# Kernel optimization log

Hardware: AMD Instinct MI355X
Metric: run time of the kernel (lower is better)

## Reference

```python
import jax, jax.numpy as jnp
import numpy as np

EMB = 2048
HEADS = 8
HEAD_DIM = EMB // HEADS  # 256

def setup_inputs() -> dict:
    key = jax.random.key(0)
    ks = jax.random.split(key, 4)
    b, n = 2, 2048
    x = jax.random.normal(ks[0], (b, n, EMB), dtype=jnp.float32)
    # Linear weights stored as [in, out] (y = x @ W + b)
    w_qkv = jax.random.normal(ks[1], (EMB, 3 * EMB), dtype=jnp.float32) * (EMB ** -0.5)
    b_qkv = jnp.zeros((3 * EMB,), dtype=jnp.float32)
    w_proj = jax.random.normal(ks[2], (EMB, EMB), dtype=jnp.float32) * (EMB ** -0.5)
    b_proj = jnp.zeros((EMB,), dtype=jnp.float32)
    return {"x": x, "w_qkv": w_qkv, "b_qkv": b_qkv, "w_proj": w_proj, "b_proj": b_proj}

def reference(x, w_qkv, b_qkv, w_proj, b_proj):
    b, n, _ = x.shape
    qkv = x @ w_qkv + b_qkv                                   # [b, n, 3*emb]
    # rearrange 'b n (h d qkv) -> qkv b h n d': qkv index is innermost
    qkv = qkv.reshape(b, n, HEADS, HEAD_DIM, 3)
    qkv = jnp.transpose(qkv, (4, 0, 2, 1, 3))                 # [3, b, h, n, d]
    q, k, v = qkv[0], qkv[1], qkv[2]
    energy = jnp.einsum('bhqd,bhkd->bhqk', q, k)              # [b, h, n, n]
    scaling = EMB ** 0.5
    # NOTE: faithful to source — softmax on UNSCALED logits, divide after.
    att = jax.nn.softmax(energy, axis=-1) / scaling
    out = jnp.einsum('bhal,bhlv->bhav', att, v)               # [b, h, n, d]
    out = jnp.transpose(out, (0, 2, 1, 3)).reshape(b, n, EMB)  # b n (h d)
    return out @ w_proj + b_proj
```

## Files before the change

kernel.cpp:

```cpp
#include <hip/hip_runtime.h>
#include <cstdint>
#include <cstddef>


typedef __bf16 bf16x8 __attribute__((ext_vector_type(8)));
typedef __bf16 bf16x2 __attribute__((ext_vector_type(2)));
typedef float f32x4 __attribute__((ext_vector_type(4)));

#define SCALE_INV 0.022097086912079608f

#define GLDS16(gp, lp)                                                        \
  __builtin_amdgcn_global_load_lds(                                           \
      (const __attribute__((address_space(1))) void*)(gp),                    \
      (__attribute__((address_space(3))) void*)(lp), 16, 0, 0)

__device__ inline void split8(const float4 v0, const float4 v1, bf16x8& hi,
                              bf16x8& lo) {
  float a[8] = {v0.x, v0.y, v0.z, v0.w, v1.x, v1.y, v1.z, v1.w};
  bf16x8 h, l;
#pragma unroll
  for (int i = 0; i < 8; i++) {
    __bf16 hh = (__bf16)a[i];
    h[i] = hh;
    l[i] = (__bf16)(a[i] - (float)hh);
  }
  hi = h;
  lo = l;
}

__global__ __launch_bounds__(256) void transpose_cvt_k(
    const float* __restrict__ in, __bf16* __restrict__ out, int R, int C) {
  __shared__ float tile[32][33];
  const int tx = threadIdx.x & 31;
  const int ty = threadIdx.x >> 5;
  const int c0 = blockIdx.x * 32;
  const int r0 = blockIdx.y * 32;
#pragma unroll
  for (int i = 0; i < 32; i += 8)
    tile[ty + i][tx] = in[(size_t)(r0 + ty + i) * C + (c0 + tx)];
  __syncthreads();
#pragma unroll
  for (int i = 0; i < 32; i += 8)
    out[(size_t)(c0 + ty + i) * R + (r0 + tx)] = (__bf16)tile[tx][ty + i];
}

__global__ __launch_bounds__(256) void transpose_w_split_k(
    const float* __restrict__ in, __bf16* __restrict__ wh,
    __bf16* __restrict__ wl1, __bf16* __restrict__ wl2) {
  __shared__ float tile[64][65];
  const int tid = threadIdx.x;
  const int c0 = blockIdx.x * 64;
  const int r0 = blockIdx.y * 64;
  const int cx = tid & 15, ry = tid >> 4;
#pragma unroll
  for (int p = 0; p < 4; p++) {
    const float4 v =
        *(const float4*)&in[(size_t)(r0 + p * 16 + ry) * 6144 + c0 + cx * 4];
    tile[p * 16 + ry][cx * 4 + 0] = v.x;
    tile[p * 16 + ry][cx * 4 + 1] = v.y;
    tile[p * 16 + ry][cx * 4 + 2] = v.z;
    tile[p * 16 + ry][cx * 4 + 3] = v.w;
  }
  __syncthreads();
  const int r2 = tid & 31;
  const int cy = tid >> 5;
  __bf16* wlb = (c0 < 2048) ? wl1 + (size_t)c0 * 2048
                            : wl2 + (size_t)(c0 - 2048) * 2048;
#pragma unroll
  for (int p = 0; p < 8; p++) {
    const int cl = cy + p * 8;
    const float t0 = tile[2 * r2][cl];
    const float t1 = tile[2 * r2 + 1][cl];
    const __bf16 h0 = (__bf16)t0, h1 = (__bf16)t1;
    bf16x2 hv = {h0, h1};
    bf16x2 lv = {(__bf16)(t0 - (float)h0), (__bf16)(t1 - (float)h1)};
    *(bf16x2*)&wh[(size_t)(c0 + cl) * 2048 + r0 + 2 * r2] = hv;
    *(bf16x2*)&wlb[(size_t)cl * 2048 + r0 + 2 * r2] = lv;
  }
}

__global__ __launch_bounds__(256) void gemm_qkv_split_k(
    const float* __restrict__ X, const __bf16* __restrict__ Wh,
    const __bf16* __restrict__ Wl1, const __bf16* __restrict__ Wl2,
    const float* __restrict__ bias, __bf16* __restrict__ qh_,
    __bf16* __restrict__ ql_, __bf16* __restrict__ kh_,
    __bf16* __restrict__ kl_, __bf16* __restrict__ vT) {
  __shared__ __bf16 Ah[2][128 * 40], Al[2][128 * 40];
  __shared__ __attribute__((aligned(16))) __bf16 BhL[2][4096];
  __shared__ __attribute__((aligned(16))) __bf16 BlL[2][4096];
  const int tid = threadIdx.x, lane = tid & 63, wave = tid >> 6;
  const int l16 = lane & 15, quad = lane >> 4;
  const int wm = (wave >> 1) * 64, wn = (wave & 1) * 64;
  const int m0 = blockIdx.y * 128, n0 = blockIdx.x * 128;
  const int r0 = tid >> 2, kc0 = (tid & 3) * 8;

  f32x4 zero4 = {0.f, 0.f, 0.f, 0.f};
  f32x4 acc[4][4];
#pragma unroll
  for (int i = 0; i < 4; i++)
#pragma unroll
    for (int j = 0; j < 4; j++) acc[i][j] = zero4;

  const float* Arow0 = X + (size_t)(m0 + r0) * 2048 + kc0;
  const float* Arow1 = Arow0 + (size_t)64 * 2048;
  const __bf16* BhP = Wh + (size_t)n0 * 2048;
  const __bf16* BlP = (n0 < 2048) ? Wl1 + (size_t)n0 * 2048
                                  : Wl2 + (size_t)(n0 - 2048) * 2048;

  const int rowl = lane >> 2, gq = lane & 3;
  const int sg = gq ^ (rowl & 3);
  size_t bSrc[2];
  int bDst[2];
#pragma unroll
  for (int i = 0; i < 2; i++) {
    const int row = wave * 32 + i * 16 + rowl;
    bSrc[i] = (size_t)row * 2048 + sg * 8;
    bDst[i] = (wave * 32 + i * 16) * 32;
  }
  const int bro = (wn + l16) * 32 + ((quad ^ (l16 & 3)) << 3);

  float4 a00 = *(const float4*)(Arow0);
  float4 a01 = *(const float4*)(Arow0 + 4);
  float4 a10 = *(const float4*)(Arow1);
  float4 a11 = *(const float4*)(Arow1 + 4);
  GLDS16(BhP + bSrc[0], &BhL[0][bDst[0]]);
  GLDS16(BhP + bSrc[1], &BhL[0][bDst[1]]);
  GLDS16(BlP + bSrc[0], &BlL[0][bDst[0]]);
  GLDS16(BlP + bSrc[1], &BlL[0][bDst[1]]);
  bf16x8 ah0, al0, ah1, al1;
  split8(a00, a01, ah0, al0);
  split8(a10, a11, ah1, al1);
  *(bf16x8*)&Ah[0][r0 * 40 + kc0] = ah0;
  *(bf16x8*)&Al[0][r0 * 40 + kc0] = al0;
  *(bf16x8*)&Ah[0][(r0 + 64) * 40 + kc0] = ah1;
  *(bf16x8*)&Al[0][(r0 + 64) * 40 + kc0] = al1;

  for (int k0 = 0; k0 < 2048; k0 += 32) {
    const int cur = (k0 >> 5) & 1;
    __syncthreads();
    const int nxt = k0 + 32;
    if (nxt < 2048) {
      a00 = *(const float4*)(Arow0 + nxt);
      a01 = *(const float4*)(Arow0 + nxt + 4);
      a10 = *(const float4*)(Arow1 + nxt);
      a11 = *(const float4*)(Arow1 + nxt + 4);
      GLDS16(BhP + bSrc[0] + nxt, &BhL[cur ^ 1][bDst[0]]);
      GLDS16(BhP + bSrc[1] + nxt, &BhL[cur ^ 1][bDst[1]]);
      GLDS16(BlP + bSrc[0] + nxt, &BlL[cur ^ 1][bDst[0]]);
      GLDS16(BlP + bSrc[1] + nxt, &BlL[cur ^ 1][bDst[1]]);
    }
    bf16x8 fah[4], fal[4], fbh[4], fbl[4];
#pragma unroll
    for (int i = 0; i < 4; i++) {
      fah[i] = *(const bf16x8*)&Ah[cur][(wm + i * 16 + l16) * 40 + quad * 8];
      fal[i] = *(const bf16x8*)&Al[cur][(wm + i * 16 + l16) * 40 + quad * 8];
    }
#pragma unroll
    for (int j = 0; j < 4; j++) {
      fbh[j] = *(const bf16x8*)&BhL[cur][bro + j * 512];
      fbl[j] = *(const bf16x8*)&BlL[cur][bro + j * 512];
    }
#pragma unroll
    for (int i = 0; i < 4; i++)
#pragma unroll
      for (int j = 0; j < 4; j++) {
        acc[i][j] = __builtin_amdgcn_mfma_f32_16x16x32_bf16(fah[i], fbh[j],
                                                            acc[i][j], 0, 0, 0);
        acc[i][j] = __builtin_amdgcn_mfma_f32_16x16x32_bf16(fah[i], fbl[j],
                                                            acc[i][j], 0, 0, 0);
        acc[i][j] = __builtin_amdgcn_mfma_f32_16x16x32_bf16(fal[i], fbh[j],
                                                            acc[i][j], 0, 0, 0);
      }
    if (nxt < 2048) {
      split8(a00, a01, ah0, al0);
      split8(a10, a11, ah1, al1);
      *(bf16x8*)&Ah[cur ^ 1][r0 * 40 + kc0] = ah0;
      *(bf16x8*)&Al[cur ^ 1][r0 * 40 + kc0] = al0;
      *(bf16x8*)&Ah[cur ^ 1][(r0 + 64) * 40 + kc0] = ah1;
      *(bf16x8*)&Al[cur ^ 1][(r0 + 64) * 40 + kc0] = al1;
    }
  }

#pragma unroll
  for (int i = 0; i < 4; i++) {
#pragma unroll
    for (int j = 0; j < 4; j++) {
      const int col = n0 + wn + j * 16 + l16;
      const float bv = bias[col];
      const int h = col / 768;
      const int rr = col - h * 768;
      const int d = rr / 3;
      const int c = rr - d * 3;
#pragma unroll
      for (int r = 0; r < 4; r++) {
        const int row = m0 + wm + i * 16 + quad * 4 + r;
        const float v = acc[i][j][r] + bv;
        const int b = row >> 11;
        const int nn = row & 2047;
        const int bh = b * 8 + h;
        const size_t idx = ((size_t)bh * 2048 + nn) * 256 + d;
        if (c == 0) {
          __bf16 hi = (__bf16)v;
          qh_[idx] = hi;
          ql_[idx] = (__bf16)(v - (float)hi);
        } else if (c == 1) {
          __bf16 hi = (__bf16)v;
          kh_[idx] = hi;
          kl_[idx] = (__bf16)(v - (float)hi);
        } else {
          vT[((size_t)bh * 256 + d) * 2048 + nn] = (__bf16)v;
        }
      }
    }
  }
}

__global__ __launch_bounds__(256, 2) void attn_fwd_k(
    const __bf16* __restrict__ Qh,
    const __bf16* __restrict__ Ql,
    const __bf16* __restrict__ Kh,
    const __bf16* __restrict__ Kl,
    const __bf16* __restrict__ Vt,
    __bf16* __restrict__ out) {
  __shared__ __attribute__((aligned(16))) __bf16 KhL[64 * 256];
  __shared__ __attribute__((aligned(16))) __bf16 KlL[64 * 256];
  __shared__ __attribute__((aligned(16))) __bf16 Plds[4][16 * 72];

  const int qblk = blockIdx.x;
  const int bh = blockIdx.y;
  const int bb = bh >> 3, hh = bh & 7;
  const int tid = threadIdx.x, lane = tid & 63, wave = tid >> 6;
  const int l16 = lane & 15, quad = lane >> 4;

  const size_t hqk = (size_t)bh * 2048 * 256;
  const __bf16* qhp = Qh + hqk;
  const __bf16* qlp = Ql + hqk;
  const __bf16* khp = Kh + hqk;
  const __bf16* klp = Kl + hqk;
  const __bf16* vp = Vt + (size_t)bh * 256 * 2048;

  const int qrow = qblk * 64 + wave * 16;

  bf16x8 qhf[8], qlf[8];
#pragma unroll
  for (int t = 0; t < 8; t++) {
    const size_t off = (size_t)(qrow + l16) * 256 + t * 32 + quad * 8;
    qhf[t] = *(const bf16x8*)&qhp[off];
    qlf[t] = *(const bf16x8*)&qlp[off];
  }

  f32x4 zero4 = {0.f, 0.f, 0.f, 0.f};
  f32x4 o[16];
#pragma unroll
  for (int dt = 0; dt < 16; dt++) o[dt] = zero4;
  float mrow[4], lrow[4];
#pragma unroll
  for (int r = 0; r < 4; r++) {
    mrow[r] = -3.0e38f;
    lrow[r] = 0.f;
  }

  int koff[8];
#pragma unroll
  for (int i = 0; i < 8; i++) {
    const int r = wave * 16 + i * 2 + (lane >> 5);
    const int cb = ((lane & 31) << 4) ^ ((r & 7) << 4);
    koff[i] = r * 256 + (cb >> 1);
  }
  const int ldsb = wave * 4096;

#pragma unroll
  for (int i = 0; i < 8; i++) {
    GLDS16(khp + koff[i], &KhL[ldsb + i * 512]);
    GLDS16(klp + koff[i], &KlL[ldsb + i * 512]);
  }

  for (int kv0 = 0; kv0 < 2048; kv0 += 64) {
    __syncthreads();

    f32x4 s[4];
#pragma unroll
    for (int j = 0; j < 4; j++) s[j] = zero4;
    __builtin_amdgcn_s_setprio(1);
#pragma unroll
    for (int j = 0; j < 4; j++) {
      const int row = j * 16 + l16;
      const int swz = (row & 7) << 3;
      const int rb = row * 256;
#pragma unroll
      for (int t = 0; t < 8; t++) {
        const int off = rb + ((t * 32 + quad * 8) ^ swz);
        bf16x8 khf = *(const bf16x8*)&KhL[off];
        bf16x8 klf = *(const bf16x8*)&KlL[off];
        s[j] =
            __builtin_amdgcn_mfma_f32_16x16x32_bf16(qhf[t], khf, s[j], 0, 0, 0);
        s[j] =
            __builtin_amdgcn_mfma_f32_16x16x32_bf16(qhf[t], klf, s[j], 0, 0, 0);
        s[j] =
            __builtin_amdgcn_mfma_f32_16x16x32_bf16(qlf[t], khf, s[j], 0, 0, 0);
      }
    }
    __builtin_amdgcn_s_setprio(0);
    __syncthreads();

    if (kv0 + 64 < 2048) {
      const int kvn = (kv0 + 64) * 256;
#pragma unroll
      for (int i = 0; i < 8; i++) {
        GLDS16(khp + kvn + koff[i], &KhL[ldsb + i * 512]);
        GLDS16(klp + kvn + koff[i], &KlL[ldsb + i * 512]);
      }
    }

    float mnew[4], alpha[4], psum[4];
#pragma unroll
    for (int r = 0; r < 4; r++) {
      float mx = fmaxf(fmaxf(s[0][r], s[1][r]), fmaxf(s[2][r], s[3][r]));
#pragma unroll
      for (int off = 1; off < 16; off <<= 1)
        mx = fmaxf(mx, __shfl_xor(mx, off, 16));
      mnew[r] = fmaxf(mrow[r], mx);
      alpha[r] = __expf(mrow[r] - mnew[r]);
      psum[r] = 0.f;
    }
#pragma unroll
    for (int j = 0; j < 4; j++)
#pragma unroll
      for (int r = 0; r < 4; r++) {
        float p = __expf(s[j][r] - mnew[r]);
        s[j][r] = p;
        psum[r] += p;
      }
#pragma unroll
    for (int r = 0; r < 4; r++) {
#pragma unroll
      for (int off = 1; off < 16; off <<= 1)
        psum[r] += __shfl_xor(psum[r], off, 16);
      lrow[r] = lrow[r] * alpha[r] + psum[r];
      mrow[r] = mnew[r];
    }
#pragma unroll
    for (int dt = 0; dt < 16; dt++) {
      o[dt][0] *= alpha[0];
      o[dt][1] *= alpha[1];
      o[dt][2] *= alpha[2];
      o[dt][3] *= alpha[3];
    }
#pragma unroll
    for (int j = 0; j < 4; j++)
#pragma unroll
      for (int r = 0; r < 4; r++)
        Plds[wave][(quad * 4 + r) * 72 + j * 16 + l16] = (__bf16)s[j][r];
    bf16x8 pa0 = *(const bf16x8*)&Plds[wave][l16 * 72 + quad * 8];
    bf16x8 pa1 = *(const bf16x8*)&Plds[wave][l16 * 72 + 32 + quad * 8];

    __builtin_amdgcn_s_setprio(1);
#pragma unroll
    for (int dt = 0; dt < 16; dt++) {
      const __bf16* vr = vp + (size_t)(dt * 16 + l16) * 2048 + kv0 + quad * 8;
      bf16x8 vf0 = *(const bf16x8*)vr;
      bf16x8 vf1 = *(const bf16x8*)(vr + 32);
      o[dt] = __builtin_amdgcn_mfma_f32_16x16x32_bf16(pa0, vf0, o[dt], 0, 0, 0);
      o[dt] = __builtin_amdgcn_mfma_f32_16x16x32_bf16(pa1, vf1, o[dt], 0, 0, 0);
    }
    __builtin_amdgcn_s_setprio(0);
  }

#pragma unroll
  for (int r = 0; r < 4; r++) {
    const float inv = SCALE_INV / lrow[r];
    const int n = qrow + quad * 4 + r;
    const size_t base = ((size_t)bb * 2048 + n) * 2048 + hh * 256;
#pragma unroll
    for (int dt = 0; dt < 16; dt++)
      out[base + dt * 16 + l16] = (__bf16)(o[dt][r] * inv);
  }
}

__global__ __launch_bounds__(256) void gemm_bt_k(
    const __bf16* __restrict__ A, const __bf16* __restrict__ Bt,
    const float* __restrict__ bias, int M, int Ncols, int K,
    float* __restrict__ outF) {
  __shared__ __bf16 As[128 * 40];
  __shared__ __bf16 Bs[128 * 40];
  const int tid = threadIdx.x, lane = tid & 63, wave = tid >> 6;
  const int l16 = lane & 15, quad = lane >> 4;
  const int wm = (wave >> 1) * 64, wn = (wave & 1) * 64;
  const int m0 = blockIdx.y * 128, n0 = blockIdx.x * 128;
  const int r0 = tid >> 2, kc0 = (tid & 3) * 8;

  f32x4 zero4 = {0.f, 0.f, 0.f, 0.f};
  f32x4 acc[4][4];
#pragma unroll
  for (int i = 0; i < 4; i++)
#pragma unroll
    for (int j = 0; j < 4; j++) acc[i][j] = zero4;

  const __bf16* Aptr = A + (size_t)(m0 + r0) * K + kc0;
  const __bf16* Bptr = Bt + (size_t)(n0 + r0) * K + kc0;
  const size_t rowstep = (size_t)64 * K;

  for (int k0 = 0; k0 < K; k0 += 32) {
    uint4 a0 = *(const uint4*)(Aptr + k0);
    uint4 a1 = *(const uint4*)(Aptr + rowstep + k0);
    uint4 b0 = *(const uint4*)(Bptr + k0);
    uint4 b1 = *(const uint4*)(Bptr + rowstep + k0);
    __syncthreads();
    *(uint4*)&As[r0 * 40 + kc0] = a0;
    *(uint4*)&As[(r0 + 64) * 40 + kc0] = a1;
    *(uint4*)&Bs[r0 * 40 + kc0] = b0;
    *(uint4*)&Bs[(r0 + 64) * 40 + kc0] = b1;
    __syncthreads();
    bf16x8 af[4], bfv[4];
#pragma unroll
    for (int i = 0; i < 4; i++)
      af[i] = *(const bf16x8*)&As[(wm + i * 16 + l16) * 40 + quad * 8];
#pragma unroll
    for (int j = 0; j < 4; j++)
      bfv[j] = *(const bf16x8*)&Bs[(wn + j * 16 + l16) * 40 + quad * 8];
#pragma unroll
    for (int i = 0; i < 4; i++)
#pragma unroll
      for (int j = 0; j < 4; j++)
        acc[i][j] = __builtin_amdgcn_mfma_f32_16x16x32_bf16(af[i], bfv[j],
                                                            acc[i][j], 0, 0, 0);
  }

#pragma unroll
  for (int i = 0; i < 4; i++)
#pragma unroll
    for (int j = 0; j < 4; j++) {
      const int col = n0 + wn + j * 16 + l16;
      const float bv = bias[col];
#pragma unroll
      for (int r = 0; r < 4; r++) {
        const int row = m0 + wm + i * 16 + quad * 4 + r;
        outF[(size_t)row * Ncols + col] = acc[i][j][r] + bv;
      }
    }
}

extern "C" void kernel_launch(void* const* d_in, const int* in_sizes, int n_in,
                              void* d_out, int out_size, void* d_ws,
                              size_t ws_size, hipStream_t stream) {
  const float* x = (const float*)d_in[0];
  const float* w_qkv = (const float*)d_in[1];
  const float* b_qkv = (const float*)d_in[2];
  const float* w_proj = (const float*)d_in[3];
  const float* b_proj = (const float*)d_in[4];
  float* out = (float*)d_out;

  const size_t HSZ = (size_t)16 * 2048 * 256;
  __bf16* qh = (__bf16*)d_ws;
  __bf16* ql = qh + HSZ;
  __bf16* kh = ql + HSZ;
  __bf16* kl = kh + HSZ;
  __bf16* vT = kl + HSZ;
  __bf16* attn = vT + HSZ;
  __bf16* wprojT = qh;

  __bf16* wh = (__bf16*)out;
  __bf16* wl1 = wh + (size_t)6144 * 2048;
  __bf16* wl2 = attn;

  transpose_w_split_k<<<dim3(96, 32), 256, 0, stream>>>(w_qkv, wh, wl1, wl2);
  gemm_qkv_split_k<<<dim3(48, 32), 256, 0, stream>>>(x, wh, wl1, wl2, b_qkv,
                                                     qh, ql, kh, kl, vT);
  attn_fwd_k<<<dim3(32, 16), 256, 0, stream>>>(qh, ql, kh, kl, vT, attn);
  transpose_cvt_k<<<dim3(64, 64), 256, 0, stream>>>(w_proj, wprojT, 2048, 2048);
  gemm_bt_k<<<dim3(16, 32), 256, 0, stream>>>(attn, wprojT, b_proj, 4096, 2048,
                                              2048, out);
}
```

Baseline: 973.7 us.

## Pre-split X into bf16 hi/lo and stream QKV GEMM operands via LDS DMA

```diff
diff --git a/kernel.cpp b/kernel.cpp
--- a/kernel.cpp
+++ b/kernel.cpp
@@ -26,6 +26,18 @@
   }
   hi = h;
   lo = l;
+}
+
+__global__ __launch_bounds__(256) void presplit_x_k(
+    const float* __restrict__ X, __bf16* __restrict__ Xh,
+    __bf16* __restrict__ Xl) {
+  const size_t i = ((size_t)blockIdx.x * 256 + threadIdx.x) * 8;
+  const float4 v0 = *(const float4*)&X[i];
+  const float4 v1 = *(const float4*)&X[i + 4];
+  bf16x8 h, l;
+  split8(v0, v1, h, l);
+  *(bf16x8*)&Xh[i] = h;
+  *(bf16x8*)&Xl[i] = l;
 }
 
 __global__ __launch_bounds__(256) void transpose_cvt_k(
@@ -46,10 +58,10 @@
 
 __global__ __launch_bounds__(256) void transpose_w_split_k(
     const float* __restrict__ in, __bf16* __restrict__ wh,
-    __bf16* __restrict__ wl1, __bf16* __restrict__ wl2) {
+    __bf16* __restrict__ wl, int col0) {
   __shared__ float tile[64][65];
   const int tid = threadIdx.x;
-  const int c0 = blockIdx.x * 64;
+  const int c0 = col0 + blockIdx.x * 64;
   const int r0 = blockIdx.y * 64;
   const int cx = tid & 15, ry = tid >> 4;
 #pragma unroll
@@ -64,8 +76,7 @@
   __syncthreads();
   const int r2 = tid & 31;
   const int cy = tid >> 5;
-  __bf16* wlb = (c0 < 2048) ? wl1 + (size_t)c0 * 2048
-                            : wl2 + (size_t)(c0 - 2048) * 2048;
+  const int cbase = c0 - col0;
 #pragma unroll
   for (int p = 0; p < 8; p++) {
     const int cl = cy + p * 8;
@@ -74,25 +85,25 @@
     const __bf16 h0 = (__bf16)t0, h1 = (__bf16)t1;
     bf16x2 hv = {h0, h1};
     bf16x2 lv = {(__bf16)(t0 - (float)h0), (__bf16)(t1 - (float)h1)};
-    *(bf16x2*)&wh[(size_t)(c0 + cl) * 2048 + r0 + 2 * r2] = hv;
-    *(bf16x2*)&wlb[(size_t)cl * 2048 + r0 + 2 * r2] = lv;
-  }
-}
-
-__global__ __launch_bounds__(256) void gemm_qkv_split_k(
-    const float* __restrict__ X, const __bf16* __restrict__ Wh,
-    const __bf16* __restrict__ Wl1, const __bf16* __restrict__ Wl2,
-    const float* __restrict__ bias, __bf16* __restrict__ qh_,
+    *(bf16x2*)&wh[(size_t)(cbase + cl) * 2048 + r0 + 2 * r2] = hv;
+    *(bf16x2*)&wl[(size_t)(cbase + cl) * 2048 + r0 + 2 * r2] = lv;
+  }
+}
+
+__global__ __launch_bounds__(256) void gemm_qkv_dma_k(
+    const __bf16* __restrict__ Xh, const __bf16* __restrict__ Xl,
+    const __bf16* __restrict__ Wh, const __bf16* __restrict__ Wl,
+    const float* __restrict__ bias, int nbase, __bf16* __restrict__ qh_,
     __bf16* __restrict__ ql_, __bf16* __restrict__ kh_,
     __bf16* __restrict__ kl_, __bf16* __restrict__ vT) {
-  __shared__ __bf16 Ah[2][128 * 40], Al[2][128 * 40];
+  __shared__ __attribute__((aligned(16))) __bf16 AhL[2][4096];
+  __shared__ __attribute__((aligned(16))) __bf16 AlL[2][4096];
   __shared__ __attribute__((aligned(16))) __bf16 BhL[2][4096];
   __shared__ __attribute__((aligned(16))) __bf16 BlL[2][4096];
   const int tid = threadIdx.x, lane = tid & 63, wave = tid >> 6;
   const int l16 = lane & 15, quad = lane >> 4;
   const int wm = (wave >> 1) * 64, wn = (wave & 1) * 64;
   const int m0 = blockIdx.y * 128, n0 = blockIdx.x * 128;
-  const int r0 = tid >> 2, kc0 = (tid & 3) * 8;
 
   f32x4 zero4 = {0.f, 0.f, 0.f, 0.f};
   f32x4 acc[4][4];
@@ -101,59 +112,48 @@
 #pragma unroll
     for (int j = 0; j < 4; j++) acc[i][j] = zero4;
 
-  const float* Arow0 = X + (size_t)(m0 + r0) * 2048 + kc0;
-  const float* Arow1 = Arow0 + (size_t)64 * 2048;
-  const __bf16* BhP = Wh + (size_t)n0 * 2048;
-  const __bf16* BlP = (n0 < 2048) ? Wl1 + (size_t)n0 * 2048
-                                  : Wl2 + (size_t)(n0 - 2048) * 2048;
-
   const int rowl = lane >> 2, gq = lane & 3;
   const int sg = gq ^ (rowl & 3);
-  size_t bSrc[2];
-  int bDst[2];
+  size_t srcOff[2];
+  int dst[2];
 #pragma unroll
   for (int i = 0; i < 2; i++) {
     const int row = wave * 32 + i * 16 + rowl;
-    bSrc[i] = (size_t)row * 2048 + sg * 8;
-    bDst[i] = (wave * 32 + i * 16) * 32;
-  }
+    srcOff[i] = (size_t)row * 2048 + sg * 8;
+    dst[i] = (wave * 32 + i * 16) * 32;
+  }
+  const __bf16* AhG = Xh + (size_t)m0 * 2048;
+  const __bf16* AlG = Xl + (size_t)m0 * 2048;
+  const __bf16* BhG = Wh + (size_t)n0 * 2048;
+  const __bf16* BlG = Wl + (size_t)n0 * 2048;
+
+  const int aro = (wm + l16) * 32 + ((quad ^ (l16 & 3)) << 3);
   const int bro = (wn + l16) * 32 + ((quad ^ (l16 & 3)) << 3);
 
-  float4 a00 = *(const float4*)(Arow0);
-  float4 a01 = *(const float4*)(Arow0 + 4);
-  float4 a10 = *(const float4*)(Arow1);
-  float4 a11 = *(const float4*)(Arow1 + 4);
-  GLDS16(BhP + bSrc[0], &BhL[0][bDst[0]]);
-  GLDS16(BhP + bSrc[1], &BhL[0][bDst[1]]);
-  GLDS16(BlP + bSrc[0], &BlL[0][bDst[0]]);
-  GLDS16(BlP + bSrc[1], &BlL[0][bDst[1]]);
-  bf16x8 ah0, al0, ah1, al1;
-  split8(a00, a01, ah0, al0);
-  split8(a10, a11, ah1, al1);
-  *(bf16x8*)&Ah[0][r0 * 40 + kc0] = ah0;
-  *(bf16x8*)&Al[0][r0 * 40 + kc0] = al0;
-  *(bf16x8*)&Ah[0][(r0 + 64) * 40 + kc0] = ah1;
-  *(bf16x8*)&Al[0][(r0 + 64) * 40 + kc0] = al1;
+#define STAGEQ(buf, koff)                                                     \
+  do {                                                                        \
+    GLDS16(AhG + srcOff[0] + (koff), &AhL[buf][dst[0]]);                      \
+    GLDS16(AhG + srcOff[1] + (koff), &AhL[buf][dst[1]]);                      \
+    GLDS16(AlG + srcOff[0] + (koff), &AlL[buf][dst[0]]);                      \
+    GLDS16(AlG + srcOff[1] + (koff), &AlL[buf][dst[1]]);                      \
+    GLDS16(BhG + srcOff[0] + (koff), &BhL[buf][dst[0]]);                      \
+    GLDS16(BhG + srcOff[1] + (koff), &BhL[buf][dst[1]]);                      \
+    GLDS16(BlG + srcOff[0] + (koff), &BlL[buf][dst[0]]);                      \
+    GLDS16(BlG + srcOff[1] + (koff), &BlL[buf][dst[1]]);                      \
+  } while (0)
+
+  STAGEQ(0, 0);
 
   for (int k0 = 0; k0 < 2048; k0 += 32) {
     const int cur = (k0 >> 5) & 1;
     __syncthreads();
     const int nxt = k0 + 32;
-    if (nxt < 2048) {
-      a00 = *(const float4*)(Arow0 + nxt);
-      a01 = *(const float4*)(Arow0 + nxt + 4);
-      a10 = *(const float4*)(Arow1 + nxt);
-      a11 = *(const float4*)(Arow1 + nxt + 4);
-      GLDS16(BhP + bSrc[0] + nxt, &BhL[cur ^ 1][bDst[0]]);
-      GLDS16(BhP + bSrc[1] + nxt, &BhL[cur ^ 1][bDst[1]]);
-      GLDS16(BlP + bSrc[0] + nxt, &BlL[cur ^ 1][bDst[0]]);
-      GLDS16(BlP + bSrc[1] + nxt, &BlL[cur ^ 1][bDst[1]]);
-    }
+    if (nxt < 2048) STAGEQ(cur ^ 1, nxt);
     bf16x8 fah[4], fal[4], fbh[4], fbl[4];
 #pragma unroll
     for (int i = 0; i < 4; i++) {
-      fah[i] = *(const bf16x8*)&Ah[cur][(wm + i * 16 + l16) * 40 + quad * 8];
-      fal[i] = *(const bf16x8*)&Al[cur][(wm + i * 16 + l16) * 40 + quad * 8];
+      fah[i] = *(const bf16x8*)&AhL[cur][aro + i * 512];
+      fal[i] = *(const bf16x8*)&AlL[cur][aro + i * 512];
     }
 #pragma unroll
     for (int j = 0; j < 4; j++) {
@@ -171,21 +171,14 @@
         acc[i][j] = __builtin_amdgcn_mfma_f32_16x16x32_bf16(fal[i], fbh[j],
                                                             acc[i][j], 0, 0, 0);
       }
-    if (nxt < 2048) {
-      split8(a00, a01, ah0, al0);
-      split8(a10, a11, ah1, al1);
-      *(bf16x8*)&Ah[cur ^ 1][r0 * 40 + kc0] = ah0;
-      *(bf16x8*)&Al[cur ^ 1][r0 * 40 + kc0] = al0;
-      *(bf16x8*)&Ah[cur ^ 1][(r0 + 64) * 40 + kc0] = ah1;
-      *(bf16x8*)&Al[cur ^ 1][(r0 + 64) * 40 + kc0] = al1;
-    }
-  }
+  }
+#undef STAGEQ
 
 #pragma unroll
   for (int i = 0; i < 4; i++) {
 #pragma unroll
     for (int j = 0; j < 4; j++) {
-      const int col = n0 + wn + j * 16 + l16;
+      const int col = nbase + n0 + wn + j * 16 + l16;
       const float bv = bias[col];
       const int h = col / 768;
       const int rr = col - h * 768;
@@ -459,13 +452,18 @@
   __bf16* attn = vT + HSZ;
   __bf16* wprojT = qh;
 
-  __bf16* wh = (__bf16*)out;
-  __bf16* wl1 = wh + (size_t)6144 * 2048;
-  __bf16* wl2 = attn;
-
-  transpose_w_split_k<<<dim3(96, 32), 256, 0, stream>>>(w_qkv, wh, wl1, wl2);
-  gemm_qkv_split_k<<<dim3(48, 32), 256, 0, stream>>>(x, wh, wl1, wl2, b_qkv,
-                                                     qh, ql, kh, kl, vT);
+  __bf16* xh = (__bf16*)out;
+  __bf16* xl = xh + (size_t)4096 * 2048;
+  __bf16* wsp_h = attn;
+  __bf16* wsp_l = wsp_h + (size_t)2048 * 2048;
+
+  presplit_x_k<<<dim3(4096), 256, 0, stream>>>(x, xh, xl);
+  for (int ph = 0; ph < 3; ph++) {
+    transpose_w_split_k<<<dim3(32, 32), 256, 0, stream>>>(w_qkv, wsp_h, wsp_l,
+                                                          ph * 2048);
+    gemm_qkv_dma_k<<<dim3(16, 32), 256, 0, stream>>>(
+        xh, xl, wsp_h, wsp_l, b_qkv, ph * 2048, qh, ql, kh, kl, vT);
+  }
   attn_fwd_k<<<dim3(32, 16), 256, 0, stream>>>(qh, ql, kh, kl, vT, attn);
   transpose_cvt_k<<<dim3(64, 64), 256, 0, stream>>>(w_proj, wprojT, 2048, 2048);
   gemm_bt_k<<<dim3(16, 32), 256, 0, stream>>>(attn, wprojT, b_proj, 4096, 2048,
```

Result: faster. 891.6 us (-8.4%).
